# Kernel tuning notes

Measured on AMD Instinct MI355X. Metric: run time of the kernel, lower is better.

## Reference

```python
import jax, jax.numpy as jnp
import numpy as np

IN_FEATURES = 4096
LOCAL_FEATURES = 128
KERNEL_SIZE = 64
STRIDE = 32
FOLD_NUM = (IN_FEATURES - KERNEL_SIZE) // STRIDE + 1  # 127
BATCH = 4096


def setup_inputs() -> dict:
    key = jax.random.key(0)
    kx, kw, kb = jax.random.split(key, 3)
    x = jax.random.normal(kx, (BATCH, IN_FEATURES), dtype=jnp.float32)
    # Per-window linear weights: torch Linear weight is [out, in] = [local_features, kernel_size]
    bound = 1.0 / np.sqrt(KERNEL_SIZE)
    W = jax.random.uniform(kw, (FOLD_NUM, LOCAL_FEATURES, KERNEL_SIZE),
                           dtype=jnp.float32, minval=-bound, maxval=bound)
    b = jax.random.uniform(kb, (FOLD_NUM, LOCAL_FEATURES),
                           dtype=jnp.float32, minval=-bound, maxval=bound)
    return {"x": x, "W": W, "b": b}


def reference(x, W, b) -> jnp.ndarray:
    # Unfold: windows[f, k] = x[:, f*stride + k] -> [B, FOLD_NUM, KERNEL_SIZE]
    idx = jnp.arange(FOLD_NUM)[:, None] * STRIDE + jnp.arange(KERNEL_SIZE)[None, :]
    windows = x[:, idx]  # [B, F, K]
    # Batched per-window linear: out[b, f, l] = sum_k windows[b,f,k] * W[f,l,k] + b[f,l]
    out = jnp.einsum('bfk,flk->bfl', windows, W) + b[None, :, :]
    # torch.cat along dim 1 over fold index == reshape [B, F*L]
    return out.reshape(x.shape[0], FOLD_NUM * LOCAL_FEATURES)
```

## Files before the change

kernel.cpp:

```cpp
#include <hip/hip_runtime.h>
#include <hip/hip_bf16.h>

#define IN_F 4096
#define LOCAL_F 128
#define KSZ 64
#define STRIDE_ 32
#define FOLDS 127
#define BATCH_ 4096
#define OUT_F (FOLDS * LOCAL_F)
#define WN (FOLDS * LOCAL_F * KSZ)

#define BM 64
#define NF 2
#define XCOLS (NF * STRIDE_ + (KSZ - STRIDE_))
#define LDSP 104

typedef __attribute__((ext_vector_type(8))) short bf16x8;
typedef __attribute__((ext_vector_type(8))) unsigned short u16x8;
typedef __attribute__((ext_vector_type(4))) float f32x4;

__device__ __forceinline__ unsigned short f2bf(float f) {
    unsigned u = __builtin_bit_cast(unsigned, f);
    u += 0x7fffu + ((u >> 16) & 1u);
    return (unsigned short)(u >> 16);
}

__global__ __launch_bounds__(256)
void wprep_kernel(const float* __restrict__ W, unsigned short* __restrict__ Wbf) {
    int i = (blockIdx.x * 256 + threadIdx.x) * 8;
    if (i >= WN) return;
    float4 a = *reinterpret_cast<const float4*>(W + i);
    float4 c = *reinterpret_cast<const float4*>(W + i + 4);
    u16x8 s;
    s[0] = f2bf(a.x); s[1] = f2bf(a.y); s[2] = f2bf(a.z); s[3] = f2bf(a.w);
    s[4] = f2bf(c.x); s[5] = f2bf(c.y); s[6] = f2bf(c.z); s[7] = f2bf(c.w);
    *reinterpret_cast<u16x8*>(Wbf + i) = s;
}

__global__ __launch_bounds__(256, 4)
void local_linear_kernel(const float* __restrict__ x,
                         const unsigned short* __restrict__ Wbf,
                         const float* __restrict__ b,
                         float* __restrict__ out) {
    __shared__ unsigned short xs[BM][LDSP];

    const int bg = blockIdx.x;
    const int fg = blockIdx.y;
    const int row0 = bg * BM;
    const int col0 = fg * (NF * STRIDE_);

    const int t = threadIdx.x;

    #pragma unroll
    for (int it = 0; it < (BM * (XCOLS / 4)) / 256; ++it) {
        int i  = t + it * 256;
        int r  = i / (XCOLS / 4);
        int c4 = i - r * (XCOLS / 4);
        int gcol = col0 + c4 * 4;
        float4 v = make_float4(0.f, 0.f, 0.f, 0.f);
        if (gcol < IN_F) {
            v = *reinterpret_cast<const float4*>(x + (size_t)(row0 + r) * IN_F + gcol);
        }
        ushort4 s;
        s.x = f2bf(v.x); s.y = f2bf(v.y); s.z = f2bf(v.z); s.w = f2bf(v.w);
        *reinterpret_cast<ushort4*>(&xs[r][c4 * 4]) = s;
    }
    __syncthreads();

    const int wave = t >> 6;
    const int lane = t & 63;
    const int fold = wave >> 1;
    const int h    = wave & 1;
    const int f = fg * NF + fold;
    if (f >= FOLDS) return;

    const int l16 = lane & 15;
    const int g   = lane >> 4;

    f32x4 acc[4][4];
    #pragma unroll
    for (int mt = 0; mt < 4; ++mt)
        #pragma unroll
        for (int nt = 0; nt < 4; ++nt)
            acc[mt][nt] = (f32x4){0.f, 0.f, 0.f, 0.f};

    const int fcol = fold * STRIDE_;
    const unsigned short* Wf = Wbf + (size_t)f * (LOCAL_F * KSZ) + (h * 4 * 16) * KSZ;

    #pragma unroll
    for (int ks = 0; ks < 2; ++ks) {
        bf16x8 wf[4];
        #pragma unroll
        for (int nt = 0; nt < 4; ++nt)
            wf[nt] = *reinterpret_cast<const bf16x8*>(Wf + (nt * 16 + l16) * KSZ + ks * 32 + g * 8);
        bf16x8 af[4];
        #pragma unroll
        for (int mt = 0; mt < 4; ++mt)
            af[mt] = *reinterpret_cast<const bf16x8*>(&xs[mt * 16 + l16][fcol + ks * 32 + g * 8]);
        #pragma unroll
        for (int mt = 0; mt < 4; ++mt)
            #pragma unroll
            for (int nt = 0; nt < 4; ++nt)
                acc[mt][nt] = __builtin_amdgcn_mfma_f32_16x16x32_bf16(wf[nt], af[mt], acc[mt][nt], 0, 0, 0);
    }

    f32x4 bv[4];
    #pragma unroll
    for (int nt = 0; nt < 4; ++nt)
        bv[nt] = *reinterpret_cast<const f32x4*>(b + (size_t)f * LOCAL_F + h * 64 + nt * 16 + 4 * g);

    #pragma unroll
    for (int mt = 0; mt < 4; ++mt) {
        float* orow = out + (size_t)(row0 + mt * 16 + l16) * OUT_F + f * LOCAL_F + h * 64 + 4 * g;
        #pragma unroll
        for (int nt = 0; nt < 4; ++nt) {
            f32x4 v = acc[mt][nt] + bv[nt];
            __builtin_nontemporal_store(v, reinterpret_cast<f32x4*>(orow + nt * 16));
        }
    }
}

extern "C" void kernel_launch(void* const* d_in, const int* in_sizes, int n_in,
                              void* d_out, int out_size, void* d_ws, size_t ws_size,
                              hipStream_t stream) {
    const float* x = (const float*)d_in[0];
    const float* W = (const float*)d_in[1];
    const float* b = (const float*)d_in[2];
    float* out = (float*)d_out;
    unsigned short* Wbf = (unsigned short*)d_ws;

    wprep_kernel<<<(WN / 8 + 255) / 256, 256, 0, stream>>>(W, Wbf);
    dim3 grid(BATCH_ / BM, (FOLDS + NF - 1) / NF);
    local_linear_kernel<<<grid, 256, 0, stream>>>(x, Wbf, b, out);
}
```

Measured before the change: 103.0 us.

## Pre-convert x to bf16 in workspace and load MFMA operands directly from global

Adds a separate pass that converts all of x to bf16 in the workspace. The main kernel then drops its LDS staging, in-kernel conversion and barrier, and loads A fragments straight from global bf16 x. All operand loads for both k-steps are issued up front, before the MFMA loop. In exchange it pays an extra full read of x in fp32 plus a write and re-read of a bf16 copy (32 MB of extra traffic), and overlapping window loads now go through cache rather than shared memory.

New measurement: 110.6 us. 1.07x slower.

```diff
diff --git a/kernel.cpp b/kernel.cpp
--- a/kernel.cpp
+++ b/kernel.cpp
@@ -9,11 +9,7 @@
 #define BATCH_ 4096
 #define OUT_F (FOLDS * LOCAL_F)
 #define WN (FOLDS * LOCAL_F * KSZ)
-
-#define BM 64
-#define NF 2
-#define XCOLS (NF * STRIDE_ + (KSZ - STRIDE_))
-#define LDSP 104
+#define XN (BATCH_ * IN_F)
 
 typedef __attribute__((ext_vector_type(8))) short bf16x8;
 typedef __attribute__((ext_vector_type(8))) unsigned short u16x8;
@@ -26,56 +22,49 @@
 }
 
 __global__ __launch_bounds__(256)
-void wprep_kernel(const float* __restrict__ W, unsigned short* __restrict__ Wbf) {
+void cvt_kernel(const float* __restrict__ src, unsigned short* __restrict__ dst, int n) {
     int i = (blockIdx.x * 256 + threadIdx.x) * 8;
-    if (i >= WN) return;
-    float4 a = *reinterpret_cast<const float4*>(W + i);
-    float4 c = *reinterpret_cast<const float4*>(W + i + 4);
+    if (i >= n) return;
+    float4 a = *reinterpret_cast<const float4*>(src + i);
+    float4 c = *reinterpret_cast<const float4*>(src + i + 4);
     u16x8 s;
     s[0] = f2bf(a.x); s[1] = f2bf(a.y); s[2] = f2bf(a.z); s[3] = f2bf(a.w);
     s[4] = f2bf(c.x); s[5] = f2bf(c.y); s[6] = f2bf(c.z); s[7] = f2bf(c.w);
-    *reinterpret_cast<u16x8*>(Wbf + i) = s;
+    *reinterpret_cast<u16x8*>(dst + i) = s;
 }
 
-__global__ __launch_bounds__(256, 4)
-void local_linear_kernel(const float* __restrict__ x,
-                         const unsigned short* __restrict__ Wbf,
-                         const float* __restrict__ b,
-                         float* __restrict__ out) {
-    __shared__ unsigned short xs[BM][LDSP];
-
+__global__ __launch_bounds__(256, 3)
+void ll_main(const unsigned short* __restrict__ xbf,
+             const unsigned short* __restrict__ Wbf,
+             const float* __restrict__ b,
+             float* __restrict__ out) {
     const int bg = blockIdx.x;
     const int fg = blockIdx.y;
-    const int row0 = bg * BM;
-    const int col0 = fg * (NF * STRIDE_);
+    const int row0 = bg * 64;
 
-    const int t = threadIdx.x;
-
-    #pragma unroll
-    for (int it = 0; it < (BM * (XCOLS / 4)) / 256; ++it) {
-        int i  = t + it * 256;
-        int r  = i / (XCOLS / 4);
-        int c4 = i - r * (XCOLS / 4);
-        int gcol = col0 + c4 * 4;
-        float4 v = make_float4(0.f, 0.f, 0.f, 0.f);
-        if (gcol < IN_F) {
-            v = *reinterpret_cast<const float4*>(x + (size_t)(row0 + r) * IN_F + gcol);
-        }
-        ushort4 s;
-        s.x = f2bf(v.x); s.y = f2bf(v.y); s.z = f2bf(v.z); s.w = f2bf(v.w);
-        *reinterpret_cast<ushort4*>(&xs[r][c4 * 4]) = s;
-    }
-    __syncthreads();
-
-    const int wave = t >> 6;
-    const int lane = t & 63;
+    const int wave = threadIdx.x >> 6;
+    const int lane = threadIdx.x & 63;
     const int fold = wave >> 1;
     const int h    = wave & 1;
-    const int f = fg * NF + fold;
+    const int f = fg * 2 + fold;
     if (f >= FOLDS) return;
 
     const int l16 = lane & 15;
     const int g   = lane >> 4;
+
+    const unsigned short* Wf = Wbf + ((size_t)f * LOCAL_F + h * 64) * KSZ;
+    const unsigned short* xw = xbf + (size_t)row0 * IN_F + f * STRIDE_;
+
+    bf16x8 wf[2][4], af[2][4];
+    #pragma unroll
+    for (int ks = 0; ks < 2; ++ks) {
+        #pragma unroll
+        for (int nt = 0; nt < 4; ++nt)
+            wf[ks][nt] = *reinterpret_cast<const bf16x8*>(Wf + (nt * 16 + l16) * KSZ + ks * 32 + g * 8);
+        #pragma unroll
+        for (int mt = 0; mt < 4; ++mt)
+            af[ks][mt] = *reinterpret_cast<const bf16x8*>(xw + (size_t)(mt * 16 + l16) * IN_F + ks * 32 + g * 8);
+    }
 
     f32x4 acc[4][4];
     #pragma unroll
@@ -84,25 +73,13 @@
         for (int nt = 0; nt < 4; ++nt)
             acc[mt][nt] = (f32x4){0.f, 0.f, 0.f, 0.f};
 
-    const int fcol = fold * STRIDE_;
-    const unsigned short* Wf = Wbf + (size_t)f * (LOCAL_F * KSZ) + (h * 4 * 16) * KSZ;
-
     #pragma unroll
-    for (int ks = 0; ks < 2; ++ks) {
-        bf16x8 wf[4];
-        #pragma unroll
-        for (int nt = 0; nt < 4; ++nt)
-            wf[nt] = *reinterpret_cast<const bf16x8*>(Wf + (nt * 16 + l16) * KSZ + ks * 32 + g * 8);
-        bf16x8 af[4];
-        #pragma unroll
-        for (int mt = 0; mt < 4; ++mt)
-            af[mt] = *reinterpret_cast<const bf16x8*>(&xs[mt * 16 + l16][fcol + ks * 32 + g * 8]);
+    for (int ks = 0; ks < 2; ++ks)
         #pragma unroll
         for (int mt = 0; mt < 4; ++mt)
             #pragma unroll
             for (int nt = 0; nt < 4; ++nt)
-                acc[mt][nt] = __builtin_amdgcn_mfma_f32_16x16x32_bf16(wf[nt], af[mt], acc[mt][nt], 0, 0, 0);
-    }
+                acc[mt][nt] = __builtin_amdgcn_mfma_f32_16x16x32_bf16(wf[ks][nt], af[ks][mt], acc[mt][nt], 0, 0, 0);
 
     f32x4 bv[4];
     #pragma unroll
@@ -127,9 +104,13 @@
     const float* W = (const float*)d_in[1];
     const float* b = (const float*)d_in[2];
     float* out = (float*)d_out;
-    unsigned short* Wbf = (unsigned short*)d_ws;
 
-    wprep_kernel<<<(WN / 8 + 255) / 256, 256, 0, stream>>>(W, Wbf);
-    dim3 grid(BATCH_ / BM, (FOLDS + NF - 1) / NF);
-    local_linear_kernel<<<grid, 256, 0, stream>>>(x, Wbf, b, out);
+    unsigned short* xbf = (unsigned short*)d_ws;
+    unsigned short* Wbf = (unsigned short*)d_ws + XN;
+
+    cvt_kernel<<<(XN / 8 + 255) / 256, 256, 0, stream>>>(x, xbf, XN);
+    cvt_kernel<<<(WN / 8 + 255) / 256, 256, 0, stream>>>(W, Wbf, WN);
+
+    dim3 grid(BATCH_ / 64, 64);
+    ll_main<<<grid, 256, 0, stream>>>(xbf, Wbf, b, out);
 }
```
